# Performance work log

Measured on AMD Instinct MI355X. Metric: run time of the kernel, lower is better.

The kernel has to match this reference:

```python
import jax, jax.numpy as jnp
import numpy as np

MC = 16384
IND_T = 96
N_MAT = 4
N_STRIKES = 21


def _init_linear(key, fan_in, fan_out, prefix=()):
    k1, k2 = jax.random.split(key)
    lim = 1.0 / np.sqrt(fan_in)
    W = jax.random.uniform(k1, prefix + (fan_in, fan_out), minval=-lim, maxval=lim, dtype=jnp.float32)
    b = jax.random.uniform(k2, prefix + (fan_out,), minval=-lim, maxval=lim, dtype=jnp.float32)
    return W, b


def setup_inputs() -> dict:
    key = jax.random.key(0)
    ks = jax.random.split(key, 14)
    z = jax.random.normal(ks[0], (MC, IND_T), dtype=jnp.float32)
    zz = jax.random.normal(ks[1], (MC, IND_T), dtype=jnp.float32)
    timegrid = jnp.arange(IND_T + 1, dtype=jnp.float32) / 365.0  # daily grid
    maturities = jnp.array([24, 48, 72, 96], dtype=jnp.int32)    # in days
    strikes = jnp.linspace(0.8, 1.2, N_STRIKES, dtype=jnp.float32)
    sv_W1, sv_b1 = _init_linear(ks[2], 3, 100)
    sv_W2, sv_b2 = _init_linear(ks[3], 100, 100)
    sv_W3, sv_b3 = _init_linear(ks[4], 100, 1)
    vh_W1, vh_b1 = _init_linear(ks[5], 2, 20, (N_MAT,))
    vh_W2, vh_b2 = _init_linear(ks[6], 20, N_STRIKES, (N_MAT,))
    vd_W1, vd_b1 = _init_linear(ks[7], 1, 20)
    vd_W2, vd_b2 = _init_linear(ks[8], 20, 1)
    vv_W1, vv_b1 = _init_linear(ks[9], 1, 20)
    vv_W2, vv_b2 = _init_linear(ks[10], 20, 1)
    v0 = jax.random.uniform(ks[11], (1,), dtype=jnp.float32) * 0.1
    rho = jnp.ones((1,), dtype=jnp.float32) * -2.0
    return dict(S0=jnp.float32(1.0), rate=jnp.float32(0.05), z=z, zz=zz,
                timegrid=timegrid, strikes=strikes, v0=v0, rho=rho,
                sv_W1=sv_W1, sv_b1=sv_b1, sv_W2=sv_W2, sv_b2=sv_b2, sv_W3=sv_W3, sv_b3=sv_b3,
                vh_W1=vh_W1, vh_b1=vh_b1, vh_W2=vh_W2, vh_b2=vh_b2,
                vd_W1=vd_W1, vd_b1=vd_b1, vd_W2=vd_W2, vd_b2=vd_b2,
                vv_W1=vv_W1, vv_b1=vv_b1, vv_W2=vv_W2, vv_b2=vv_b2,
                maturities=maturities)


def reference(S0, rate, z, zz, timegrid, strikes, v0, rho,
              sv_W1, sv_b1, sv_W2, sv_b2, sv_W3, sv_b3,
              vh_W1, vh_b1, vh_W2, vh_b2,
              vd_W1, vd_b1, vd_W2, vd_b2,
              vv_W1, vv_b1, vv_W2, vv_b2,
              maturities):
    sg = jax.lax.stop_gradient
    mc = z.shape[0]
    n_mat = vh_W1.shape[0]
    n_strikes = strikes.shape[0]

    def s_vol(x):  # [MC,3] -> [MC,1], softplus output
        h1 = jax.nn.relu(x @ sv_W1 + sv_b1)
        h2 = jax.nn.relu(h1 @ sv_W2 + sv_b2)
        return jax.nn.softplus(h2 @ sv_W3 + sv_b3)

    def v_drift(v):  # [MC,1] -> [MC,1]
        return jax.nn.relu(v @ vd_W1 + vd_b1) @ vd_W2 + vd_b2

    def v_vol(v):  # [MC,1] -> [MC,1], softplus output
        return jax.nn.softplus(jax.nn.relu(v @ vv_W1 + vv_b1) @ vv_W2 + vv_b2)

    def vanilla_hedge_all(x):  # [MC,2] -> [MC, n_strikes, n_mat] (one net per maturity)
        h1 = jax.nn.relu(jnp.einsum('mi,kio->kmo', x, vh_W1) + vh_b1[:, None, :])
        out = jax.nn.softplus(jnp.einsum('kmo,koj->kmj', h1, vh_W2) + vh_b2[:, None, :])
        return jnp.transpose(out, (1, 2, 0))

    rho_t = jnp.tanh(rho)[0]
    days = jnp.round(timegrid * 365.0).astype(jnp.int32)       # [IND_T+1]
    le = days[1:, None] <= maturities[None, :]                  # [IND_T, n_mat]
    idx_net = jnp.argmax(le, axis=1)                            # first live maturity per step
    is_mat = jnp.any(days[1:, None] == maturities[None, :], axis=1)
    mat_idx = jnp.arange(n_mat)

    Slog0 = jnp.log(jnp.full((mc, 1), S0, dtype=jnp.float32))
    V0 = jnp.full((mc, 1), 1.0, dtype=jnp.float32) * jax.nn.sigmoid(v0)[0] * 0.5
    cv0 = jnp.zeros((mc, n_strikes, n_mat), dtype=jnp.float32)
    pv0 = jnp.zeros((n_mat, n_strikes), dtype=jnp.float32)

    xs = (z.T[:, :, None], zz.T[:, :, None], timegrid[:-1], timegrid[1:], idx_net, is_mat)

    def step(carry, x):
        Slog_old, V_old, cv, pv_h, pv_var = carry
        z_i, zz_i, t0, t1, idx, im = x
        h = t1 - t0
        sqh = jnp.sqrt(h)
        dW = sqh * z_i                                          # [MC,1]
        dB = rho_t * dW + jnp.sqrt(1.0 - rho_t ** 2) * sqh * zz_i
        ones_t = jnp.full((mc, 1), 1.0, dtype=jnp.float32) * t0
        pd = s_vol(jnp.concatenate([ones_t, Slog_old, V_old], axis=1))  # price diffusion
        cv_fwd = vanilla_hedge_all(jnp.concatenate([ones_t, sg(Slog_old)], axis=1))
        V_new = V_old + v_drift(V_old) * h + v_vol(V_old) * dB
        drift = rate - 0.5 * pd ** 2
        diff = pd * dW
        drift_c = 1.0 + jnp.abs(sg(drift)) * sqh                # tamed Euler
        diff_c = 1.0 + jnp.abs(sg(pd)) * sqh
        Slog_new = Slog_old + drift * h / drift_c + diff / diff_c
        S_new = jnp.exp(Slog_new)
        S_old = jnp.exp(Slog_old)
        dS = jnp.exp(-rate * t1) * S_new - jnp.exp(-rate * t0) * S_old  # [MC,1]
        mask = (mat_idx >= idx).astype(cv.dtype)                # live maturities only
        cv = cv + mask[None, None, :] * cv_fwd * sg(dS)[:, :, None]
        # hedged vanilla (call) prices collected at maturity steps
        payoff = jnp.exp(-rate * t1) * jnp.maximum(S_new - strikes[None, :], 0.0)
        price = payoff - cv[:, :, idx]                          # [MC, n_strikes]
        pv = jnp.mean(price, axis=0)
        pvar = jnp.var(price, axis=0, ddof=1)
        sel = (mat_idx == idx)[:, None] & im
        pv_h = jnp.where(sel, pv[None, :], pv_h)
        pv_var = jnp.where(sel, pvar[None, :], pv_var)
        return (Slog_new, V_new, cv, pv_h, pv_var), None

    (_, _, _, pv_h, pv_var), _ = jax.lax.scan(step, (Slog0, V0, cv0, pv0, pv0), xs)
    return jnp.stack([pv_h, pv_var])  # [2, n_mat, n_strikes]
```

## Files before the change

### kernel.cpp

```cpp
#include <hip/hip_runtime.h>
#include <hip/hip_bf16.h>
#include <math.h>


#define MC      16384
#define NSTEP   96
#define BLOCK   256
#define NGROUP  1024
#define NPAIR   84

typedef short bf16x8 __attribute__((ext_vector_type(8)));
typedef float f32x4  __attribute__((ext_vector_type(4)));

union U8 { uint4 u; bf16x8 v; };
union BF2U { __hip_bfloat162 b; unsigned u; };

__device__ __forceinline__ unsigned bf16rne(float x) {
    unsigned u = __float_as_uint(x);
    return (u + 0x7FFFu + ((u >> 16) & 1u)) >> 16;
}
__device__ __forceinline__ unsigned pk2(float lo, float hi) {
    BF2U t; t.b = __float22bfloat162_rn(make_float2(lo, hi));
    return t.u;
}
__device__ __forceinline__ float sp(float x) {
    return fmaxf(x, 0.f) + __logf(1.f + __expf(-fabsf(x)));
}

__global__ __launch_bounds__(BLOCK, 4)
void lsv_sim(const float* __restrict__ S0p,   const float* __restrict__ ratep,
             const float* __restrict__ z,     const float* __restrict__ zzg,
             const float* __restrict__ strikesg,
             const float* __restrict__ v0p,   const float* __restrict__ rhop,
             const float* __restrict__ svW1,  const float* __restrict__ svb1,
             const float* __restrict__ svW2,  const float* __restrict__ svb2,
             const float* __restrict__ svW3,  const float* __restrict__ svb3,
             const float* __restrict__ vhW1,  const float* __restrict__ vhb1,
             const float* __restrict__ vhW2,  const float* __restrict__ vhb2,
             const float* __restrict__ vdW1,  const float* __restrict__ vdb1,
             const float* __restrict__ vdW2,  const float* __restrict__ vdb2,
             const float* __restrict__ vvW1,  const float* __restrict__ vvb1,
             const float* __restrict__ vvW2,  const float* __restrict__ vvb2,
             const int*   __restrict__ mats,
             float* __restrict__ psum, float* __restrict__ psq)
{
    __shared__ __align__(16) unsigned short H1c[16 * 16 * 8];
    __shared__ __align__(16) float W1f[16 * 32];
    __shared__ __align__(16) float WH1f[16 * 32];
    __shared__ __align__(16) float B2T[128], W3T[128];
    __shared__ __align__(16) float RED[16 * 4];
    __shared__ float VDb[16], VVb[16];
    __shared__ float PSs[32], PSq[32];
    __shared__ __align__(16) float VW[128];
    __shared__ __align__(16) float4 STEP[NSTEP];
    __shared__ float D1T[NSTEP];
    __shared__ int   ITAB[NSTEP];
    __shared__ float ZT[16][97], ZZT[16][97];
    __shared__ float SLOG[16], VST[16], SST[16], SLOGP[16], DSP[16];
    __shared__ __align__(16) float CW1[2][128];
    __shared__ __align__(16) float CH[2][128];

    const int tid  = threadIdx.x;
    const int lane = tid & 63;
    const int w    = __builtin_amdgcn_readfirstlane(tid >> 6);
    const int quad = lane >> 4;
    const int col  = lane & 15;

    const int hm   = w;
    const int path = col;
    const int kc   = w * 4 + quad;

    {
        const size_t gbase = (size_t)blockIdx.x * 16 * NSTEP;
        for (int e = tid; e < 16 * NSTEP; e += BLOCK) {
            const int p = e / NSTEP, ii = e - p * NSTEP;
            ZT[p][ii]  = z  [gbase + e];
            ZZT[p][ii] = zzg[gbase + e];
        }
    }
    for (int e = tid; e < 128; e += BLOCK) {
        float v = 0.f;
        if      (e < 20)             v = vdW1[e];
        else if (e < 40)             v = vdb1[e - 20];
        else if (e < 60)             v = vdW2[e - 40];
        else if (e >= 64 && e < 84)  v = vvW1[e - 64];
        else if (e >= 84 && e < 104) v = vvb1[e - 84];
        else if (e >= 104 && e < 124)v = vvW2[e - 104];
        else if (e == 124)           v = vdb2[0];
        else if (e == 125)           v = vvb2[0];
        VW[e] = v;
        B2T[e] = (e < 100) ? svb2[e] : 0.f;
        W3T[e] = (e < 100) ? svW3[e] : 0.f;
    }
    for (int e = tid; e < 512; e += BLOCK) {
        const int kc2 = e >> 5, r5 = e & 31, grp = r5 >> 3, kk = kc2 * 8 + (r5 & 7);
        float v = 0.f;
        if (kk < 100) v = (grp == 0) ? svW1[kk] : (grp == 1) ? svW1[100 + kk]
                        : (grp == 2) ? svW1[200 + kk] : svb1[kk];
        W1f[e] = v;
    }
    for (int e = tid; e < 512; e += BLOCK) {
        const int hq = e >> 5, r5 = e & 31, grp = r5 >> 3;
        const int hmm = hq >> 2, qq = hq & 3;
        const int j = qq * 8 + (r5 & 7);
        float v = 0.f;
        if (j < 20 && grp < 3)
            v = (grp == 0) ? vhW1[hmm * 40 + j] : (grp == 1) ? vhW1[hmm * 40 + 20 + j]
                                                : vhb1[hmm * 20 + j];
        WH1f[e] = v;
    }

    const float rate  = ratep[0];
    const float S0    = S0p[0];
    const float rho_t = tanhf(rhop[0]);
    const float srho  = sqrtf(1.f - rho_t * rho_t);
    const float b3    = svb3[0];

    if (tid < NSTEP) {
        const int i = tid;
        const float t0 = (float)i       * (1.f / 365.f);
        const float t1 = (float)(i + 1) * (1.f / 365.f);
        const float h  = t1 - t0;
        STEP[i] = make_float4(t0, h, sqrtf(h), __expf(-rate * t0));
        D1T[i]  = __expf(-rate * t1);
        const int day = i + 1;
        const int m0 = mats[0], m1 = mats[1], m2 = mats[2], m3 = mats[3];
        const int idx = (day > m0) + (day > m1) + (day > m2);
        const int mi  = (idx == 0) ? m0 : (idx == 1) ? m1 : (idx == 2) ? m2 : m3;
        ITAB[i] = idx | ((day == mi) ? 256 : 0);
    }

    bf16x8 Af[4][2];
#pragma unroll
    for (int c = 0; c < 4; c++)
#pragma unroll
        for (int t = 0; t < 2; t++) {
            U8 tt;
#pragma unroll
            for (int e2 = 0; e2 < 4; e2++) {
                const int k0 = 32 * c + 8 * quad + 2 * e2;
                const int j  = (2 * w + t) * 16 + col;
                const float v0 = (k0     < 100 && j < 100) ? svW2[k0 * 100 + j]       : 0.f;
                const float v1 = (k0 + 1 < 100 && j < 100) ? svW2[(k0 + 1) * 100 + j] : 0.f;
                (&tt.u.x)[e2] = bf16rne(v0) | (bf16rne(v1) << 16);
            }
            Af[c][t] = tt.v;
        }
    bf16x8 Ah[2];
#pragma unroll
    for (int st = 0; st < 2; st++) {
        U8 tt;
#pragma unroll
        for (int e2 = 0; e2 < 4; e2++) {
            const int j0 = 8 * quad + 2 * e2, j1 = j0 + 1;
            const int s  = st * 16 + col;
            const float v0 = (j0 < 20 && s < 21) ? vhW2[hm * 420 + j0 * 21 + s] : 0.f;
            const float v1 = (j1 < 20 && s < 21) ? vhW2[hm * 420 + j1 * 21 + s] : 0.f;
            (&tt.u.x)[e2] = bf16rne(v0) | (bf16rne(v1) << 16);
        }
        Ah[st] = tt.v;
    }
    f32x4 c0h, c1h;
    float K0a[4], K1a[4];
#pragma unroll
    for (int r = 0; r < 4; r++) {
        const int s0 = quad * 4 + r, s1 = 16 + quad * 4 + r;
        c0h[r] = vhb2[hm * 21 + s0];
        K0a[r] = strikesg[s0];
        c1h[r] = (s1 < 21) ? vhb2[hm * 21 + s1] : 0.f;
        K1a[r] = (s1 < 21) ? strikesg[s1] : 1e30f;
    }

    const float Slog0 = __logf(S0);
    const float S0v   = __expf(Slog0);
    const float V0v   = (1.f / (1.f + __expf(-v0p[0]))) * 0.5f;
    f32x4 cv0 = {0.f, 0.f, 0.f, 0.f};
    f32x4 cv1 = {0.f, 0.f, 0.f, 0.f};

    __syncthreads();

    if (tid < 128) {
        const float t00 = STEP[0].x;
        const int kk = tid;
        CW1[0][kk] = fmaf(t00, W1f[(kk >> 3) * 32 + (kk & 7)],
                               W1f[(kk >> 3) * 32 + 24 + (kk & 7)]);
    } else {
        const float t00 = STEP[0].x;
        const int e = tid - 128;
        CH[0][e] = fmaf(t00, WH1f[(e >> 3) * 32 + (e & 7)],
                             WH1f[(e >> 3) * 32 + 16 + (e & 7)]);
    }
    if (tid < 16) {
        SLOG[tid] = Slog0;
        SST[tid]  = S0v;
        VST[tid]  = V0v;
    }

    __syncthreads();

    const int j0e = (2 * w) * 16 + quad * 4;
    const float4 b2a = *reinterpret_cast<const float4*>(B2T + j0e);
    const float4 w3a = *reinterpret_cast<const float4*>(W3T + j0e);
    const float4 b2b = *reinterpret_cast<const float4*>(B2T + j0e + 16);
    const float4 w3b = *reinterpret_cast<const float4*>(W3T + j0e + 16);
    const float4 wsA = *reinterpret_cast<const float4*>(WH1f + (hm * 4 + quad) * 32 + 8);
    const float4 wsB = *reinterpret_cast<const float4*>(WH1f + (hm * 4 + quad) * 32 + 12);

    auto hedge_step = [&](int ip) {
        const int iv   = ITAB[ip];
        const int idxp = iv & 0xff;
        if (hm >= idxp) {
            const int hb = ip & 1;
            const float slp = SLOGP[path];
            U8 b;
            {
                const float4 ch4 = *reinterpret_cast<const float4*>(&CH[hb][(hm * 4 + quad) * 8]);
                (&b.u.x)[0] = pk2(fmaxf(ch4.x + slp * wsA.x, 0.f),
                                  fmaxf(ch4.y + slp * wsA.y, 0.f));
                (&b.u.x)[1] = pk2(fmaxf(ch4.z + slp * wsA.z, 0.f),
                                  fmaxf(ch4.w + slp * wsA.w, 0.f));
            }
            {
                const float4 ch4 = *reinterpret_cast<const float4*>(&CH[hb][(hm * 4 + quad) * 8 + 4]);
                (&b.u.x)[2] = pk2(fmaxf(ch4.x + slp * wsB.x, 0.f),
                                  fmaxf(ch4.y + slp * wsB.y, 0.f));
                (&b.u.x)[3] = pk2(fmaxf(ch4.z + slp * wsB.z, 0.f),
                                  fmaxf(ch4.w + slp * wsB.w, 0.f));
            }
            const f32x4 D0 = __builtin_amdgcn_mfma_f32_16x16x32_bf16(Ah[0], b.v, c0h, 0, 0, 0);
            const f32x4 D1 = __builtin_amdgcn_mfma_f32_16x16x32_bf16(Ah[1], b.v, c1h, 0, 0, 0);
            const float dsP = DSP[path];
#pragma unroll
            for (int r = 0; r < 4; r++) {
                cv0[r] += sp(D0[r]) * dsP;
                cv1[r] += sp(D1[r]) * dsP;
            }
            if ((iv & 256) && hm == idxp) {
                const float Sp  = SST[path];
                const float d1p = D1T[ip];
                float p0[4], q0[4], p1[4], q1[4];
#pragma unroll
                for (int r = 0; r < 4; r++) {
                    p0[r] = d1p * fmaxf(Sp - K0a[r], 0.f) - cv0[r];
                    p1[r] = d1p * fmaxf(Sp - K1a[r], 0.f) - cv1[r];
                    q0[r] = p0[r] * p0[r];
                    q1[r] = p1[r] * p1[r];
                }
#pragma unroll
                for (int o = 1; o <= 8; o <<= 1) {
#pragma unroll
                    for (int r = 0; r < 4; r++) {
                        p0[r] += __shfl_xor(p0[r], o);
                        q0[r] += __shfl_xor(q0[r], o);
                        p1[r] += __shfl_xor(p1[r], o);
                        q1[r] += __shfl_xor(q1[r], o);
                    }
                }
                if (col == 0) {
#pragma unroll
                    for (int r = 0; r < 4; r++) {
                        const int s0 = quad * 4 + r, s1 = 16 + quad * 4 + r;
                        PSs[s0] = p0[r];  PSq[s0] = q0[r];
                        if (s1 < 21) { PSs[s1] = p1[r];  PSq[s1] = q1[r]; }
                    }
                }
            }
        }
    };

    auto ps_reduce = [&](int ip) {
        if (w == 0) {
            const int iv = ITAB[ip];
            if (iv & 256) {
                const int s = lane & 31;
                if (s < 21) {
                    const float* src = (lane >= 32) ? &PSq[0] : &PSs[0];
                    const float acc = src[s];
                    float* dst = (lane >= 32) ? psq : psum;
                    dst[((iv & 0xff) * 21 + s) * NGROUP + blockIdx.x] = acc;
                }
            }
        }
    };

    for (int i = 0; i < NSTEP; i++) {
        const int buf = i & 1;

        {
            const float slp = SLOG[path];
            const float vp  = VST[path];
            const float* Wp = W1f + kc * 32;
            uint4 o;
#pragma unroll
            for (int hh = 0; hh < 2; hh++) {
                const float4 b4 = *reinterpret_cast<const float4*>(Wp + 8 + hh * 4);
                const float4 c4 = *reinterpret_cast<const float4*>(Wp + 16 + hh * 4);
                const float4 cw = *reinterpret_cast<const float4*>(&CW1[buf][kc * 8 + hh * 4]);
                const float x0 = fmaxf(cw.x + slp * b4.x + vp * c4.x, 0.f);
                const float x1 = fmaxf(cw.y + slp * b4.y + vp * c4.y, 0.f);
                const float x2 = fmaxf(cw.z + slp * b4.z + vp * c4.z, 0.f);
                const float x3 = fmaxf(cw.w + slp * b4.w + vp * c4.w, 0.f);
                (&o.x)[2 * hh]     = pk2(x0, x1);
                (&o.x)[2 * hh + 1] = pk2(x2, x3);
            }
            *reinterpret_cast<uint4*>(H1c + (kc * 16 + path) * 8) = o;
        }
        if (i > 0) hedge_step(i - 1);
        if (w == 1) {
            const float Vp = VST[path];
            const float* bw = VW + ((lane >= 32) ? 64 : 0);
            float a2 = 0.f;
#pragma unroll
            for (int q5 = 0; q5 < 5; q5++) {
                const float4 w1 = *reinterpret_cast<const float4*>(bw + 4 * q5);
                const float4 b1 = *reinterpret_cast<const float4*>(bw + 20 + 4 * q5);
                const float4 w2 = *reinterpret_cast<const float4*>(bw + 40 + 4 * q5);
                a2 += fmaxf(Vp * w1.x + b1.x, 0.f) * w2.x;
                a2 += fmaxf(Vp * w1.y + b1.y, 0.f) * w2.y;
                a2 += fmaxf(Vp * w1.z + b1.z, 0.f) * w2.z;
                a2 += fmaxf(Vp * w1.w + b1.w, 0.f) * w2.w;
            }
            if (quad == 0)      VDb[path] = a2;
            else if (quad == 2) VVb[path] = a2;
        }
        __syncthreads();

        {
            f32x4 d0 = {0.f, 0.f, 0.f, 0.f};
            f32x4 d1 = {0.f, 0.f, 0.f, 0.f};
#pragma unroll
            for (int c = 0; c < 4; c++) {
                const bf16x8 b = *reinterpret_cast<const bf16x8*>(
                    H1c + ((quad + 4 * c) * 16 + path) * 8);
                d0 = __builtin_amdgcn_mfma_f32_16x16x32_bf16(Af[c][0], b, d0, 0, 0, 0);
                d1 = __builtin_amdgcn_mfma_f32_16x16x32_bf16(Af[c][1], b, d1, 0, 0, 0);
            }
            float acc = fmaxf(d0[0] + b2a.x, 0.f) * w3a.x
                      + fmaxf(d0[1] + b2a.y, 0.f) * w3a.y
                      + fmaxf(d0[2] + b2a.z, 0.f) * w3a.z
                      + fmaxf(d0[3] + b2a.w, 0.f) * w3a.w
                      + fmaxf(d1[0] + b2b.x, 0.f) * w3b.x
                      + fmaxf(d1[1] + b2b.y, 0.f) * w3b.y
                      + fmaxf(d1[2] + b2b.z, 0.f) * w3b.z
                      + fmaxf(d1[3] + b2b.w, 0.f) * w3b.w;
            acc += __shfl_xor(acc, 16);
            acc += __shfl_xor(acc, 32);
            if (quad == 0)
                RED[path * 4 + w] = acc;
        }
        if (i > 0) ps_reduce(i - 1);
        __syncthreads();

        if (w == 0) {
            const int lp = lane & 15;
            const float4 rr = *reinterpret_cast<const float4*>(RED + lp * 4);
            const float pout = (rr.x + rr.y) + (rr.z + rr.w);
            const float pd = sp(pout + b3);
            const float vdv = VDb[lp] + VW[124];
            const float vvv = sp(VVb[lp] + VW[125]);
            const float4 u  = STEP[i];
            const float sqh = u.z;
            const float zi  = ZT[lp][i];
            const float zzi = ZZT[lp][i];
            const float dW = sqh * zi;
            const float dB = rho_t * dW + srho * sqh * zzi;
            const float Vold = VST[lp];
            const float Sold = SST[lp];
            const float SlogO = SLOG[lp];
            const float Vn = Vold + vdv * u.y + vvv * dB;
            const float drift   = rate - 0.5f * pd * pd;
            const float diff    = pd * dW;
            const float drift_c = 1.f + fabsf(drift) * sqh;
            const float diff_c  = 1.f + fabsf(pd) * sqh;
            const float Sln = SlogO + __fdividef(drift * u.y, drift_c) + __fdividef(diff, diff_c);
            const float Sn  = __expf(Sln);
            const float dS  = D1T[i] * Sn - u.w * Sold;
            if (lane < 16) {
                SLOGP[lp] = SlogO;  DSP[lp] = dS;
                SLOG[lp]  = Sln;    SST[lp] = Sn;  VST[lp] = Vn;
            }
        } else if (w == 2 && i + 1 < NSTEP) {
            const float t0n = STEP[i + 1].x;
#pragma unroll
            for (int rep = 0; rep < 2; rep++) {
                const int kk = rep * 64 + lane;
                CW1[buf ^ 1][kk] = fmaf(t0n, W1f[(kk >> 3) * 32 + (kk & 7)],
                                             W1f[(kk >> 3) * 32 + 24 + (kk & 7)]);
            }
        } else if (w == 3 && i + 1 < NSTEP) {
            const float t0n = STEP[i + 1].x;
#pragma unroll
            for (int rep = 0; rep < 2; rep++) {
                const int e = rep * 64 + lane;
                CH[buf ^ 1][e] = fmaf(t0n, WH1f[(e >> 3) * 32 + (e & 7)],
                                           WH1f[(e >> 3) * 32 + 16 + (e & 7)]);
            }
        }
        __syncthreads();
    }

    hedge_step(NSTEP - 1);
    __syncthreads();
    ps_reduce(NSTEP - 1);
}

__global__ void lsv_finalize(const float* __restrict__ psum,
                             const float* __restrict__ psq,
                             float* __restrict__ out)
{
    const int t    = blockIdx.x;
    const int lane = threadIdx.x;
    float s = 0.f, q = 0.f;
    for (int b = lane; b < NGROUP; b += 64) {
        s += psum[t * NGROUP + b];
        q += psq [t * NGROUP + b];
    }
#pragma unroll
    for (int o = 1; o <= 32; o <<= 1) {
        s += __shfl_xor(s, o);
        q += __shfl_xor(q, o);
    }
    if (lane == 0) {
        const float mean = s * (1.0f / (float)MC);
        const float var  = (q - (float)MC * mean * mean) * (1.0f / (float)(MC - 1));
        out[t]         = mean;
        out[NPAIR + t] = var;
    }
}

extern "C" void kernel_launch(void* const* d_in, const int* in_sizes, int n_in,
                              void* d_out, int out_size, void* d_ws, size_t ws_size,
                              hipStream_t stream)
{
    const float* S0    = (const float*)d_in[0];
    const float* rate  = (const float*)d_in[1];
    const float* z     = (const float*)d_in[2];
    const float* zz    = (const float*)d_in[3];
    const float* strikes = (const float*)d_in[5];
    const float* v0    = (const float*)d_in[6];
    const float* rho   = (const float*)d_in[7];
    const float* svW1  = (const float*)d_in[8];
    const float* svb1  = (const float*)d_in[9];
    const float* svW2  = (const float*)d_in[10];
    const float* svb2  = (const float*)d_in[11];
    const float* svW3  = (const float*)d_in[12];
    const float* svb3  = (const float*)d_in[13];
    const float* vhW1  = (const float*)d_in[14];
    const float* vhb1  = (const float*)d_in[15];
    const float* vhW2  = (const float*)d_in[16];
    const float* vhb2  = (const float*)d_in[17];
    const float* vdW1  = (const float*)d_in[18];
    const float* vdb1  = (const float*)d_in[19];
    const float* vdW2  = (const float*)d_in[20];
    const float* vdb2  = (const float*)d_in[21];
    const float* vvW1  = (const float*)d_in[22];
    const float* vvb1  = (const float*)d_in[23];
    const float* vvW2  = (const float*)d_in[24];
    const float* vvb2  = (const float*)d_in[25];
    const int*   mats  = (const int*)d_in[26];

    float* psum = (float*)d_ws;
    float* psq  = psum + NPAIR * NGROUP;

    hipLaunchKernelGGL(lsv_sim, dim3(NGROUP), dim3(BLOCK), 0, stream,
                       S0, rate, z, zz, strikes, v0, rho,
                       svW1, svb1, svW2, svb2, svW3, svb3,
                       vhW1, vhb1, vhW2, vhb2,
                       vdW1, vdb1, vdW2, vdb2,
                       vvW1, vvb1, vvW2, vvb2,
                       mats, psum, psq);

    hipLaunchKernelGGL(lsv_finalize, dim3(NPAIR), dim3(64), 0, stream,
                       psum, psq, (float*)d_out);
}
```

Baseline: 455.8 us.

## Double block to 8 waves and split MLP/hedge MFMA work per wave

Raises the block from 4 to 8 wavefronts. Each wave now computes one 16-column slice of the second-layer MLP instead of two, and each hedge maturity is split across two waves by strike half. Auxiliary tasks (the vol-drift MLP, the path update and the coefficient precompute) move to different waves, and the VDb/VVb buffers are double-buffered. The intent is to shorten the serial per-step critical path, at the cost of more waves per block and possible register pressure from launch bounds of 8.

```diff
diff --git a/kernel.cpp b/kernel.cpp
--- a/kernel.cpp
+++ b/kernel.cpp
@@ -5,7 +5,7 @@
 
 #define MC      16384
 #define NSTEP   96
-#define BLOCK   256
+#define BLOCK   512
 #define NGROUP  1024
 #define NPAIR   84
 
@@ -27,7 +27,7 @@
     return fmaxf(x, 0.f) + __logf(1.f + __expf(-fabsf(x)));
 }
 
-__global__ __launch_bounds__(BLOCK, 4)
+__global__ __launch_bounds__(BLOCK, 8)
 void lsv_sim(const float* __restrict__ S0p,   const float* __restrict__ ratep,
              const float* __restrict__ z,     const float* __restrict__ zzg,
              const float* __restrict__ strikesg,
@@ -48,8 +48,8 @@
     __shared__ __align__(16) float W1f[16 * 32];
     __shared__ __align__(16) float WH1f[16 * 32];
     __shared__ __align__(16) float B2T[128], W3T[128];
-    __shared__ __align__(16) float RED[16 * 4];
-    __shared__ float VDb[16], VVb[16];
+    __shared__ __align__(16) float RED[16 * 8];
+    __shared__ float VDb[2][16], VVb[2][16];
     __shared__ float PSs[32], PSq[32];
     __shared__ __align__(16) float VW[128];
     __shared__ __align__(16) float4 STEP[NSTEP];
@@ -66,9 +66,10 @@
     const int quad = lane >> 4;
     const int col  = lane & 15;
 
-    const int hm   = w;
+    const int mh   = w >> 1;
+    const int st   = w & 1;
     const int path = col;
-    const int kc   = w * 4 + quad;
+    const int kc   = (w & 3) * 4 + quad;
 
     {
         const size_t gbase = (size_t)blockIdx.x * 16 * NSTEP;
@@ -130,52 +131,43 @@
         ITAB[i] = idx | ((day == mi) ? 256 : 0);
     }
 
-    bf16x8 Af[4][2];
-#pragma unroll
-    for (int c = 0; c < 4; c++)
-#pragma unroll
-        for (int t = 0; t < 2; t++) {
-            U8 tt;
-#pragma unroll
-            for (int e2 = 0; e2 < 4; e2++) {
-                const int k0 = 32 * c + 8 * quad + 2 * e2;
-                const int j  = (2 * w + t) * 16 + col;
-                const float v0 = (k0     < 100 && j < 100) ? svW2[k0 * 100 + j]       : 0.f;
-                const float v1 = (k0 + 1 < 100 && j < 100) ? svW2[(k0 + 1) * 100 + j] : 0.f;
-                (&tt.u.x)[e2] = bf16rne(v0) | (bf16rne(v1) << 16);
-            }
-            Af[c][t] = tt.v;
-        }
-    bf16x8 Ah[2];
-#pragma unroll
-    for (int st = 0; st < 2; st++) {
+    bf16x8 Af[4];
+#pragma unroll
+    for (int c = 0; c < 4; c++) {
+        U8 tt;
+#pragma unroll
+        for (int e2 = 0; e2 < 4; e2++) {
+            const int k0 = 32 * c + 8 * quad + 2 * e2;
+            const int j  = w * 16 + col;
+            const float v0 = (k0     < 100 && j < 100) ? svW2[k0 * 100 + j]       : 0.f;
+            const float v1 = (k0 + 1 < 100 && j < 100) ? svW2[(k0 + 1) * 100 + j] : 0.f;
+            (&tt.u.x)[e2] = bf16rne(v0) | (bf16rne(v1) << 16);
+        }
+        Af[c] = tt.v;
+    }
+    bf16x8 Ah;
+    {
         U8 tt;
 #pragma unroll
         for (int e2 = 0; e2 < 4; e2++) {
             const int j0 = 8 * quad + 2 * e2, j1 = j0 + 1;
-            const int s  = st * 16 + col;
-            const float v0 = (j0 < 20 && s < 21) ? vhW2[hm * 420 + j0 * 21 + s] : 0.f;
-            const float v1 = (j1 < 20 && s < 21) ? vhW2[hm * 420 + j1 * 21 + s] : 0.f;
+            const int s  = (st == 0) ? col : (16 + (col & 3) * 4 + (col >> 2));
+            const float v0 = (j0 < 20 && s < 21) ? vhW2[mh * 420 + j0 * 21 + s] : 0.f;
+            const float v1 = (j1 < 20 && s < 21) ? vhW2[mh * 420 + j1 * 21 + s] : 0.f;
             (&tt.u.x)[e2] = bf16rne(v0) | (bf16rne(v1) << 16);
         }
-        Ah[st] = tt.v;
-    }
-    f32x4 c0h, c1h;
-    float K0a[4], K1a[4];
+        Ah = tt.v;
+    }
+    f32x4 c0h;
+    float K0a[4];
 #pragma unroll
     for (int r = 0; r < 4; r++) {
-        const int s0 = quad * 4 + r, s1 = 16 + quad * 4 + r;
-        c0h[r] = vhb2[hm * 21 + s0];
-        K0a[r] = strikesg[s0];
-        c1h[r] = (s1 < 21) ? vhb2[hm * 21 + s1] : 0.f;
-        K1a[r] = (s1 < 21) ? strikesg[s1] : 1e30f;
-    }
-
-    const float Slog0 = __logf(S0);
-    const float S0v   = __expf(Slog0);
-    const float V0v   = (1.f / (1.f + __expf(-v0p[0]))) * 0.5f;
+        const int s = (st == 0) ? (quad * 4 + r) : (16 + r * 4 + quad);
+        c0h[r] = (s < 21) ? vhb2[mh * 21 + s] : 0.f;
+        K0a[r] = (s < 21) ? strikesg[s] : 1e30f;
+    }
+
     f32x4 cv0 = {0.f, 0.f, 0.f, 0.f};
-    f32x4 cv1 = {0.f, 0.f, 0.f, 0.f};
 
     __syncthreads();
 
@@ -184,100 +176,117 @@
         const int kk = tid;
         CW1[0][kk] = fmaf(t00, W1f[(kk >> 3) * 32 + (kk & 7)],
                                W1f[(kk >> 3) * 32 + 24 + (kk & 7)]);
-    } else {
+    } else if (tid < 256) {
         const float t00 = STEP[0].x;
         const int e = tid - 128;
         CH[0][e] = fmaf(t00, WH1f[(e >> 3) * 32 + (e & 7)],
                              WH1f[(e >> 3) * 32 + 16 + (e & 7)]);
     }
     if (tid < 16) {
-        SLOG[tid] = Slog0;
-        SST[tid]  = S0v;
-        VST[tid]  = V0v;
+        SLOG[tid] = __logf(S0);
+        SST[tid]  = __expf(__logf(S0));
+        VST[tid]  = (1.f / (1.f + __expf(-v0p[0]))) * 0.5f;
     }
 
     __syncthreads();
 
-    const int j0e = (2 * w) * 16 + quad * 4;
+    const int j0e = w * 16 + quad * 4;
     const float4 b2a = *reinterpret_cast<const float4*>(B2T + j0e);
     const float4 w3a = *reinterpret_cast<const float4*>(W3T + j0e);
-    const float4 b2b = *reinterpret_cast<const float4*>(B2T + j0e + 16);
-    const float4 w3b = *reinterpret_cast<const float4*>(W3T + j0e + 16);
-    const float4 wsA = *reinterpret_cast<const float4*>(WH1f + (hm * 4 + quad) * 32 + 8);
-    const float4 wsB = *reinterpret_cast<const float4*>(WH1f + (hm * 4 + quad) * 32 + 12);
+    const float4 wsA = *reinterpret_cast<const float4*>(WH1f + (mh * 4 + quad) * 32 + 8);
+    const float4 wsB = *reinterpret_cast<const float4*>(WH1f + (mh * 4 + quad) * 32 + 12);
 
     auto hedge_step = [&](int ip) {
         const int iv   = ITAB[ip];
         const int idxp = iv & 0xff;
-        if (hm >= idxp) {
+        if (mh >= idxp) {
             const int hb = ip & 1;
             const float slp = SLOGP[path];
             U8 b;
             {
-                const float4 ch4 = *reinterpret_cast<const float4*>(&CH[hb][(hm * 4 + quad) * 8]);
+                const float4 ch4 = *reinterpret_cast<const float4*>(&CH[hb][(mh * 4 + quad) * 8]);
                 (&b.u.x)[0] = pk2(fmaxf(ch4.x + slp * wsA.x, 0.f),
                                   fmaxf(ch4.y + slp * wsA.y, 0.f));
                 (&b.u.x)[1] = pk2(fmaxf(ch4.z + slp * wsA.z, 0.f),
                                   fmaxf(ch4.w + slp * wsA.w, 0.f));
             }
             {
-                const float4 ch4 = *reinterpret_cast<const float4*>(&CH[hb][(hm * 4 + quad) * 8 + 4]);
+                const float4 ch4 = *reinterpret_cast<const float4*>(&CH[hb][(mh * 4 + quad) * 8 + 4]);
                 (&b.u.x)[2] = pk2(fmaxf(ch4.x + slp * wsB.x, 0.f),
                                   fmaxf(ch4.y + slp * wsB.y, 0.f));
                 (&b.u.x)[3] = pk2(fmaxf(ch4.z + slp * wsB.z, 0.f),
                                   fmaxf(ch4.w + slp * wsB.w, 0.f));
             }
-            const f32x4 D0 = __builtin_amdgcn_mfma_f32_16x16x32_bf16(Ah[0], b.v, c0h, 0, 0, 0);
-            const f32x4 D1 = __builtin_amdgcn_mfma_f32_16x16x32_bf16(Ah[1], b.v, c1h, 0, 0, 0);
+            const f32x4 D = __builtin_amdgcn_mfma_f32_16x16x32_bf16(Ah, b.v, c0h, 0, 0, 0);
             const float dsP = DSP[path];
-#pragma unroll
-            for (int r = 0; r < 4; r++) {
-                cv0[r] += sp(D0[r]) * dsP;
-                cv1[r] += sp(D1[r]) * dsP;
-            }
-            if ((iv & 256) && hm == idxp) {
+            if (st == 0) {
+#pragma unroll
+                for (int r = 0; r < 4; r++) cv0[r] += sp(D[r]) * dsP;
+            } else {
+#pragma unroll
+                for (int r = 0; r < 2; r++) cv0[r] += sp(D[r]) * dsP;
+            }
+            if ((iv & 256) && mh == idxp) {
                 const float Sp  = SST[path];
                 const float d1p = D1T[ip];
-                float p0[4], q0[4], p1[4], q1[4];
-#pragma unroll
-                for (int r = 0; r < 4; r++) {
-                    p0[r] = d1p * fmaxf(Sp - K0a[r], 0.f) - cv0[r];
-                    p1[r] = d1p * fmaxf(Sp - K1a[r], 0.f) - cv1[r];
-                    q0[r] = p0[r] * p0[r];
-                    q1[r] = p1[r] * p1[r];
+                if (st == 0) {
+                    float p0[4], q0[4];
+#pragma unroll
+                    for (int r = 0; r < 4; r++) {
+                        p0[r] = d1p * fmaxf(Sp - K0a[r], 0.f) - cv0[r];
+                        q0[r] = p0[r] * p0[r];
+                    }
+#pragma unroll
+                    for (int o = 1; o <= 8; o <<= 1) {
+#pragma unroll
+                        for (int r = 0; r < 4; r++) {
+                            p0[r] += __shfl_xor(p0[r], o);
+                            q0[r] += __shfl_xor(q0[r], o);
+                        }
+                    }
+                    if (col == 0) {
+#pragma unroll
+                        for (int r = 0; r < 4; r++) {
+                            const int s0 = quad * 4 + r;
+                            PSs[s0] = p0[r];  PSq[s0] = q0[r];
+                        }
+                    }
+                } else {
+                    float p0[2], q0[2];
+#pragma unroll
+                    for (int r = 0; r < 2; r++) {
+                        p0[r] = d1p * fmaxf(Sp - K0a[r], 0.f) - cv0[r];
+                        q0[r] = p0[r] * p0[r];
+                    }
+#pragma unroll
+                    for (int o = 1; o <= 8; o <<= 1) {
+#pragma unroll
+                        for (int r = 0; r < 2; r++) {
+                            p0[r] += __shfl_xor(p0[r], o);
+                            q0[r] += __shfl_xor(q0[r], o);
+                        }
+                    }
+                    if (col == 0) {
+#pragma unroll
+                        for (int r = 0; r < 2; r++) {
+                            const int s1 = 16 + r * 4 + quad;
+                            if (s1 < 21) { PSs[s1] = p0[r];  PSq[s1] = q0[r]; }
+                        }
+                    }
                 }
-#pragma unroll
-                for (int o = 1; o <= 8; o <<= 1) {
-#pragma unroll
-                    for (int r = 0; r < 4; r++) {
-                        p0[r] += __shfl_xor(p0[r], o);
-                        q0[r] += __shfl_xor(q0[r], o);
-                        p1[r] += __shfl_xor(p1[r], o);
-                        q1[r] += __shfl_xor(q1[r], o);
-                    }
-                }
-                if (col == 0) {
-#pragma unroll
-                    for (int r = 0; r < 4; r++) {
-                        const int s0 = quad * 4 + r, s1 = 16 + quad * 4 + r;
-                        PSs[s0] = p0[r];  PSq[s0] = q0[r];
-                        if (s1 < 21) { PSs[s1] = p1[r];  PSq[s1] = q1[r]; }
-                    }
-                }
             }
         }
     };
 
     auto ps_reduce = [&](int ip) {
-        if (w == 0) {
+        if (w == 7) {
             const int iv = ITAB[ip];
             if (iv & 256) {
                 const int s = lane & 31;
                 if (s < 21) {
                     const float* src = (lane >= 32) ? &PSq[0] : &PSs[0];
-                    const float acc = src[s];
                     float* dst = (lane >= 32) ? psq : psum;
-                    dst[((iv & 0xff) * 21 + s) * NGROUP + blockIdx.x] = acc;
+                    dst[((iv & 0xff) * 21 + s) * NGROUP + blockIdx.x] = src[s];
                 }
             }
         }
@@ -286,7 +295,7 @@
     for (int i = 0; i < NSTEP; i++) {
         const int buf = i & 1;
 
-        {
+        if (w < 4) {
             const float slp = SLOG[path];
             const float vp  = VST[path];
             const float* Wp = W1f + kc * 32;
@@ -306,9 +315,10 @@
             *reinterpret_cast<uint4*>(H1c + (kc * 16 + path) * 8) = o;
         }
         if (i > 0) hedge_step(i - 1);
-        if (w == 1) {
-            const float Vp = VST[path];
-            const float* bw = VW + ((lane >= 32) ? 64 : 0);
+        if (w == 0 && lane < 32) {
+            const int p = lane & 15;
+            const float Vp = VST[p];
+            const float* bw = VW + ((lane >= 16) ? 64 : 0);
             float a2 = 0.f;
 #pragma unroll
             for (int q5 = 0; q5 < 5; q5++) {
@@ -320,44 +330,39 @@
                 a2 += fmaxf(Vp * w1.z + b1.z, 0.f) * w2.z;
                 a2 += fmaxf(Vp * w1.w + b1.w, 0.f) * w2.w;
             }
-            if (quad == 0)      VDb[path] = a2;
-            else if (quad == 2) VVb[path] = a2;
+            if (lane < 16) VDb[buf][p] = a2; else VVb[buf][p] = a2;
         }
         __syncthreads();
 
         {
             f32x4 d0 = {0.f, 0.f, 0.f, 0.f};
-            f32x4 d1 = {0.f, 0.f, 0.f, 0.f};
 #pragma unroll
             for (int c = 0; c < 4; c++) {
                 const bf16x8 b = *reinterpret_cast<const bf16x8*>(
                     H1c + ((quad + 4 * c) * 16 + path) * 8);
-                d0 = __builtin_amdgcn_mfma_f32_16x16x32_bf16(Af[c][0], b, d0, 0, 0, 0);
-                d1 = __builtin_amdgcn_mfma_f32_16x16x32_bf16(Af[c][1], b, d1, 0, 0, 0);
+                d0 = __builtin_amdgcn_mfma_f32_16x16x32_bf16(Af[c], b, d0, 0, 0, 0);
             }
             float acc = fmaxf(d0[0] + b2a.x, 0.f) * w3a.x
                       + fmaxf(d0[1] + b2a.y, 0.f) * w3a.y
                       + fmaxf(d0[2] + b2a.z, 0.f) * w3a.z
-                      + fmaxf(d0[3] + b2a.w, 0.f) * w3a.w
-                      + fmaxf(d1[0] + b2b.x, 0.f) * w3b.x
-                      + fmaxf(d1[1] + b2b.y, 0.f) * w3b.y
-                      + fmaxf(d1[2] + b2b.z, 0.f) * w3b.z
-                      + fmaxf(d1[3] + b2b.w, 0.f) * w3b.w;
+                      + fmaxf(d0[3] + b2a.w, 0.f) * w3a.w;
             acc += __shfl_xor(acc, 16);
             acc += __shfl_xor(acc, 32);
             if (quad == 0)
-                RED[path * 4 + w] = acc;
+                RED[path * 8 + w] = acc;
         }
         if (i > 0) ps_reduce(i - 1);
         __syncthreads();
 
-        if (w == 0) {
+        if (w == 4) {
             const int lp = lane & 15;
-            const float4 rr = *reinterpret_cast<const float4*>(RED + lp * 4);
-            const float pout = (rr.x + rr.y) + (rr.z + rr.w);
+            const float4 r0 = *reinterpret_cast<const float4*>(RED + lp * 8);
+            const float4 r1 = *reinterpret_cast<const float4*>(RED + lp * 8 + 4);
+            const float pout = ((r0.x + r0.y) + (r0.z + r0.w))
+                             + ((r1.x + r1.y) + (r1.z + r1.w));
             const float pd = sp(pout + b3);
-            const float vdv = VDb[lp] + VW[124];
-            const float vvv = sp(VVb[lp] + VW[125]);
+            const float vdv = VDb[buf][lp] + VW[124];
+            const float vvv = sp(VVb[buf][lp] + VW[125]);
             const float4 u  = STEP[i];
             const float sqh = u.z;
             const float zi  = ZT[lp][i];
@@ -379,7 +384,7 @@
                 SLOGP[lp] = SlogO;  DSP[lp] = dS;
                 SLOG[lp]  = Sln;    SST[lp] = Sn;  VST[lp] = Vn;
             }
-        } else if (w == 2 && i + 1 < NSTEP) {
+        } else if (w == 5 && i + 1 < NSTEP) {
             const float t0n = STEP[i + 1].x;
 #pragma unroll
             for (int rep = 0; rep < 2; rep++) {
@@ -387,7 +392,7 @@
                 CW1[buf ^ 1][kk] = fmaf(t0n, W1f[(kk >> 3) * 32 + (kk & 7)],
                                              W1f[(kk >> 3) * 32 + 24 + (kk & 7)]);
             }
-        } else if (w == 3 && i + 1 < NSTEP) {
+        } else if (w == 6 && i + 1 < NSTEP) {
             const float t0n = STEP[i + 1].x;
 #pragma unroll
             for (int rep = 0; rep < 2; rep++) {
```

After: 1.025 ms. +125.0%, slower.
